# Optimization experiments

Hardware: AMD Instinct MI355X
Metric: run time of the kernel (lower is better)

The kernel has to match this reference:

```python
import jax, jax.numpy as jnp
import numpy as np

N_PREV = 8191
DIMS = 4096


def setup_inputs() -> dict:
    key = jax.random.key(0)
    k1, k2, k3, k4, k5 = jax.random.split(key, 5)
    prev_inps = jax.random.normal(k1, (N_PREV, DIMS), dtype=jnp.float32)
    inp = jax.random.normal(k2, (DIMS,), dtype=jnp.float32)
    # learned parameters, init std=0.01 as in the torch module
    W_Q = jax.random.normal(k3, (DIMS, DIMS), dtype=jnp.float32) * 0.01
    W_K = jax.random.normal(k4, (DIMS, DIMS), dtype=jnp.float32) * 0.01
    W_V = jax.random.normal(k5, (DIMS, DIMS), dtype=jnp.float32) * 0.01
    return {"prev_inps": prev_inps, "inp": inp, "W_Q": W_Q, "W_K": W_K, "W_V": W_V}


def reference(prev_inps, inp, W_Q, W_K, W_V):
    # One masked self-attention decode step.
    inputs = jnp.concatenate([prev_inps, inp[None, :]], axis=0)  # (n+1, d)
    query = W_Q @ inp                                            # (d,)
    keys = jnp.einsum('md,nd->nm', W_K, inputs)                  # (n+1, d)
    values = jnp.einsum('md,nd->nm', W_V, inputs)                # (n+1, d)
    logits = keys @ query                                        # (n+1,)
    aweights = jax.nn.softmax(logits, axis=-1)                   # (n+1,)
    context = aweights @ values                                  # (d,)
    output = context + inp                                       # residual
    return (output, inputs)
```

## Files before the change

### kernel.cpp

```cpp
#include <hip/hip_runtime.h>
#include <math.h>

#define D      4096
#define NPREV  8191
#define NROWS  8192
#define NWAVE  2048
#define RPW    4

typedef float f4 __attribute__((ext_vector_type(4)));

static __device__ __forceinline__ f4 nt_load4(const float* p) {
    return __builtin_nontemporal_load(reinterpret_cast<const f4*>(p));
}
static __device__ __forceinline__ f4 ld4(const float* p) {
    return *reinterpret_cast<const f4*>(p);
}
static __device__ __forceinline__ void st4(f4 v, float* p) {
    *reinterpret_cast<f4*>(p) = v;
}

template<bool RESIDUAL>
__global__ void k_matvec_rows(const float* __restrict__ W, const float* __restrict__ v,
                              const float* __restrict__ resid, float* __restrict__ out) {
    int row  = blockIdx.x * 4 + (threadIdx.x >> 6);
    int lane = threadIdx.x & 63;
    const float* Wrow = W + (size_t)row * D;
    float acc = 0.f;
    #pragma unroll
    for (int i = 0; i < 16; ++i) {
        int c = lane + i * 64;
        f4 w = nt_load4(Wrow + 4 * c);
        f4 x = ld4(v + 4 * c);
        acc += w.x * x.x + w.y * x.y + w.z * x.z + w.w * x.w;
    }
    #pragma unroll
    for (int off = 32; off; off >>= 1) acc += __shfl_down(acc, off, 64);
    if (lane == 0) out[row] = RESIDUAL ? (acc + resid[row]) : acc;
}

__global__ void k_kq(const float* __restrict__ W, const float* __restrict__ q,
                     float* __restrict__ kq) {
    __shared__ float s_q[D];
    __shared__ f4 s_part[64][4];
    int t = threadIdx.x;
    int b = blockIdx.x;
    for (int i = t; i < D; i += 256) s_q[i] = q[i];
    __syncthreads();
    int c4 = b * 4 + (t & 3);
    int r0 = t >> 2;
    f4 acc = (f4)0.f;
    #pragma unroll 16
    for (int i = 0; i < 64; ++i) {
        int m = r0 + i * 64;
        acc += s_q[m] * nt_load4(W + (size_t)m * D + 4 * c4);
    }
    s_part[r0][t & 3] = acc;
    __syncthreads();
    if (t < 4) {
        f4 a = (f4)0.f;
        #pragma unroll
        for (int g = 0; g < 64; ++g) a += s_part[g][t];
        st4(a, kq + 4 * (b * 4 + t));
    }
}

__global__ __launch_bounds__(256, 2) void k_flash_pure(
        const float* __restrict__ prev, const float* __restrict__ inp,
        const float* __restrict__ kq,
        float* __restrict__ ms, float* __restrict__ ctxpart) {
    const int t = threadIdx.x;
    const int lane = t & 63;
    const int gw = blockIdx.x * 4 + (t >> 6);

    f4 kqr[16];
    #pragma unroll
    for (int i = 0; i < 16; ++i) kqr[i] = ld4(kq + 4 * (lane + 64 * i));

    float m = -INFINITY, s = 0.f;
    f4 a[16];
    #pragma unroll
    for (int i = 0; i < 16; ++i) a[i] = (f4)0.f;

    for (int k = 0; k < RPW; ++k) {
        int n = gw + NWAVE * k;
        const float* src = (n < NPREV) ? (prev + (size_t)n * D) : inp;
        f4 x[16];
        #pragma unroll
        for (int i = 0; i < 16; ++i) x[i] = ld4(src + 4 * (lane + 64 * i));
        float p = 0.f;
        #pragma unroll
        for (int i = 0; i < 16; ++i)
            p += x[i].x * kqr[i].x + x[i].y * kqr[i].y
               + x[i].z * kqr[i].z + x[i].w * kqr[i].w;
        #pragma unroll
        for (int off = 32; off; off >>= 1) p += __shfl_down(p, off, 64);
        p = __shfl(p, 0, 64);
        if (p > m) {
            float sc = __expf(m - p);
            s *= sc;
            #pragma unroll
            for (int i = 0; i < 16; ++i) a[i] *= sc;
            m = p;
        }
        float e = __expf(p - m);
        s += e;
        #pragma unroll
        for (int i = 0; i < 16; ++i) a[i] += e * x[i];
    }
    float* cp = ctxpart + (size_t)gw * D;
    #pragma unroll
    for (int i = 0; i < 16; ++i) st4(a[i], cp + 4 * (lane + 64 * i));
    if (lane == 0) { ms[2 * gw] = m; ms[2 * gw + 1] = s; }
}

template<int FBT>
__global__ void k_combine(const float* __restrict__ ms, const float* __restrict__ ctxpart,
                          float* __restrict__ ctx) {
    constexpr int PPT = FBT / 256;
    constexpr int PPG = FBT / 16;
    __shared__ float s_w[FBT];
    __shared__ float s_red[8];
    __shared__ f4 s_acc[16][16];
    int t = threadIdx.x;
    int lane = t & 63, wid = t >> 6;
    float mloc[PPT];
    float mx = -INFINITY;
    #pragma unroll
    for (int k = 0; k < PPT; ++k) { mloc[k] = ms[2 * (t + 256 * k)]; mx = fmaxf(mx, mloc[k]); }
    #pragma unroll
    for (int off = 32; off; off >>= 1) mx = fmaxf(mx, __shfl_down(mx, off, 64));
    if (lane == 0) s_red[wid] = mx;
    __syncthreads();
    float M = fmaxf(fmaxf(s_red[0], s_red[1]), fmaxf(s_red[2], s_red[3]));
    float sc = 0.f;
    #pragma unroll
    for (int k = 0; k < PPT; ++k) {
        float w = __expf(mloc[k] - M);
        s_w[t + 256 * k] = w;
        sc += w * ms[2 * (t + 256 * k) + 1];
    }
    #pragma unroll
    for (int off = 32; off; off >>= 1) sc += __shfl_down(sc, off, 64);
    if (lane == 0) s_red[4 + wid] = sc;
    __syncthreads();
    float S = s_red[4] + s_red[5] + s_red[6] + s_red[7];
    int c = t & 15, g = t >> 4;
    int col4 = blockIdx.x * 16 + c;
    f4 a = (f4)0.f;
    #pragma unroll 8
    for (int i = 0; i < PPG; ++i) {
        int pp = g * PPG + i;
        a += s_w[pp] * ld4(ctxpart + (size_t)pp * D + 4 * col4);
    }
    s_acc[g][c] = a;
    __syncthreads();
    if (t < 16) {
        f4 aa = (f4)0.f;
        #pragma unroll
        for (int gg = 0; gg < 16; ++gg) aa += s_acc[gg][t];
        st4(aa * (1.f / S), ctx + 4 * (blockIdx.x * 16 + t));
    }
}

extern "C" void kernel_launch(void* const* d_in, const int* in_sizes, int n_in,
                              void* d_out, int out_size, void* d_ws, size_t ws_size,
                              hipStream_t stream) {
    const float* prev = (const float*)d_in[0];
    const float* inp  = (const float*)d_in[1];
    const float* W_Q  = (const float*)d_in[2];
    const float* W_K  = (const float*)d_in[3];
    const float* W_V  = (const float*)d_in[4];
    float* out = (float*)d_out;
    float* io  = out + D;
    float* ws  = (float*)d_ws;

    float* q       = ws;
    float* kq      = q + D;
    float* ms      = kq + D;
    float* ctxpart = ms + 2 * NWAVE;
    float* ctx     = ctxpart + (size_t)NWAVE * D;

    k_matvec_rows<false><<<1024, 256, 0, stream>>>(W_Q, inp, nullptr, q);
    k_kq<<<256, 256, 0, stream>>>(W_K, q, kq);

    hipMemcpyAsync(io, prev, (size_t)NPREV * D * sizeof(float),
                   hipMemcpyDeviceToDevice, stream);
    hipMemcpyAsync(io + (size_t)NPREV * D, inp, D * sizeof(float),
                   hipMemcpyDeviceToDevice, stream);

    k_flash_pure<<<512, 256, 0, stream>>>(prev, inp, kq, ms, ctxpart);

    k_combine<NWAVE><<<64, 256, 0, stream>>>(ms, ctxpart, ctx);
    k_matvec_rows<true><<<1024, 256, 0, stream>>>(W_V, ctx, inp, out);
}
```

Baseline: 132.7 us.

## Fuse the inputs copy into compute kernels as extra copy blocks

Removes the two device-to-device memcpys that write the concatenated inputs tensor. The copy is split into slices, and each of the five compute kernels gets extra leading blocks that copy one slice. The aim is to overlap the 128 MB copy traffic with the matvec, flash and combine kernels, which are latency- or underfill-bound. In exchange, copy blocks compete with compute for bandwidth and CUs, and the flash kernel's added blocks read the same prev rows at the same time as its compute blocks.

```diff
diff --git a/kernel.cpp b/kernel.cpp
--- a/kernel.cpp
+++ b/kernel.cpp
@@ -19,10 +19,26 @@
     *reinterpret_cast<f4*>(p) = v;
 }
 
+static __device__ __forceinline__ void copy_slice(
+        const float* __restrict__ prev, const float* __restrict__ inp,
+        float* __restrict__ io, size_t lo, size_t hi, int cb) {
+    const size_t stride = (size_t)cb * 256;
+    for (size_t idx = lo + (size_t)blockIdx.x * 256 + threadIdx.x;
+         idx < hi; idx += stride) {
+        f4 v = (idx < (size_t)NPREV * (D / 4))
+                 ? ld4(prev + 4 * idx)
+                 : ld4(inp + 4 * (idx - (size_t)NPREV * (D / 4)));
+        st4(v, io + 4 * idx);
+    }
+}
+
 template<bool RESIDUAL>
 __global__ void k_matvec_rows(const float* __restrict__ W, const float* __restrict__ v,
-                              const float* __restrict__ resid, float* __restrict__ out) {
-    int row  = blockIdx.x * 4 + (threadIdx.x >> 6);
+                              const float* __restrict__ resid, float* __restrict__ out,
+                              const float* __restrict__ prev, const float* __restrict__ inp,
+                              float* __restrict__ io, size_t lo, size_t hi, int cb) {
+    if ((int)blockIdx.x < cb) { copy_slice(prev, inp, io, lo, hi, cb); return; }
+    int row  = ((int)blockIdx.x - cb) * 4 + (threadIdx.x >> 6);
     int lane = threadIdx.x & 63;
     const float* Wrow = W + (size_t)row * D;
     float acc = 0.f;
@@ -39,11 +55,14 @@
 }
 
 __global__ void k_kq(const float* __restrict__ W, const float* __restrict__ q,
-                     float* __restrict__ kq) {
+                     float* __restrict__ kq,
+                     const float* __restrict__ prev, const float* __restrict__ inp,
+                     float* __restrict__ io, size_t lo, size_t hi, int cb) {
+    if ((int)blockIdx.x < cb) { copy_slice(prev, inp, io, lo, hi, cb); return; }
     __shared__ float s_q[D];
     __shared__ f4 s_part[64][4];
     int t = threadIdx.x;
-    int b = blockIdx.x;
+    int b = (int)blockIdx.x - cb;
     for (int i = t; i < D; i += 256) s_q[i] = q[i];
     __syncthreads();
     int c4 = b * 4 + (t & 3);
@@ -67,10 +86,12 @@
 __global__ __launch_bounds__(256, 2) void k_flash_pure(
         const float* __restrict__ prev, const float* __restrict__ inp,
         const float* __restrict__ kq,
-        float* __restrict__ ms, float* __restrict__ ctxpart) {
+        float* __restrict__ ms, float* __restrict__ ctxpart,
+        float* __restrict__ io, size_t lo, size_t hi, int cb) {
+    if ((int)blockIdx.x < cb) { copy_slice(prev, inp, io, lo, hi, cb); return; }
     const int t = threadIdx.x;
     const int lane = t & 63;
-    const int gw = blockIdx.x * 4 + (t >> 6);
+    const int gw = ((int)blockIdx.x - cb) * 4 + (t >> 6);
 
     f4 kqr[16];
     #pragma unroll
@@ -115,12 +136,16 @@
 
 template<int FBT>
 __global__ void k_combine(const float* __restrict__ ms, const float* __restrict__ ctxpart,
-                          float* __restrict__ ctx) {
+                          float* __restrict__ ctx,
+                          const float* __restrict__ prev, const float* __restrict__ inp,
+                          float* __restrict__ io, size_t lo, size_t hi, int cb) {
+    if ((int)blockIdx.x < cb) { copy_slice(prev, inp, io, lo, hi, cb); return; }
     constexpr int PPT = FBT / 256;
     constexpr int PPG = FBT / 16;
     __shared__ float s_w[FBT];
     __shared__ float s_red[8];
     __shared__ f4 s_acc[16][16];
+    int bb = (int)blockIdx.x - cb;
     int t = threadIdx.x;
     int lane = t & 63, wid = t >> 6;
     float mloc[PPT];
@@ -145,7 +170,7 @@
     __syncthreads();
     float S = s_red[4] + s_red[5] + s_red[6] + s_red[7];
     int c = t & 15, g = t >> 4;
-    int col4 = blockIdx.x * 16 + c;
+    int col4 = bb * 16 + c;
     f4 a = (f4)0.f;
     #pragma unroll 8
     for (int i = 0; i < PPG; ++i) {
@@ -158,7 +183,7 @@
         f4 aa = (f4)0.f;
         #pragma unroll
         for (int gg = 0; gg < 16; ++gg) aa += s_acc[gg][t];
-        st4(aa * (1.f / S), ctx + 4 * (blockIdx.x * 16 + t));
+        st4(aa * (1.f / S), ctx + 4 * (bb * 16 + t));
     }
 }
 
@@ -180,16 +205,22 @@
     float* ctxpart = ms + 2 * NWAVE;
     float* ctx     = ctxpart + (size_t)NWAVE * D;
 
-    k_matvec_rows<false><<<1024, 256, 0, stream>>>(W_Q, inp, nullptr, q);
-    k_kq<<<256, 256, 0, stream>>>(W_K, q, kq);
-
-    hipMemcpyAsync(io, prev, (size_t)NPREV * D * sizeof(float),
-                   hipMemcpyDeviceToDevice, stream);
-    hipMemcpyAsync(io + (size_t)NPREV * D, inp, D * sizeof(float),
-                   hipMemcpyDeviceToDevice, stream);
-
-    k_flash_pure<<<512, 256, 0, stream>>>(prev, inp, kq, ms, ctxpart);
-
-    k_combine<NWAVE><<<64, 256, 0, stream>>>(ms, ctxpart, ctx);
-    k_matvec_rows<true><<<1024, 256, 0, stream>>>(W_V, ctx, inp, out);
-}
+    const size_t S0 = 0;
+    const size_t S1 = 1572864;
+    const size_t S2 = 3145728;
+    const size_t S3 = 5242880;
+    const size_t S4 = 5767168;
+    const size_t S5 = 8388608;
+    const int CB1 = 256, CB2 = 256, CB3 = 256, CB4 = 128, CB5 = 512;
+
+    k_matvec_rows<false><<<CB1 + 1024, 256, 0, stream>>>(
+        W_Q, inp, nullptr, q, prev, inp, io, S0, S1, CB1);
+    k_kq<<<CB2 + 256, 256, 0, stream>>>(
+        W_K, q, kq, prev, inp, io, S1, S2, CB2);
+    k_flash_pure<<<CB3 + 512, 256, 0, stream>>>(
+        prev, inp, kq, ms, ctxpart, io, S2, S3, CB3);
+    k_combine<NWAVE><<<CB4 + 64, 256, 0, stream>>>(
+        ms, ctxpart, ctx, prev, inp, io, S3, S4, CB4);
+    k_matvec_rows<true><<<CB5 + 1024, 256, 0, stream>>>(
+        W_V, ctx, inp, out, prev, inp, io, S4, S5, CB5);
+}
```

Result: no change. 133.9 us (+0.9%).
